# Kernel tuning notes

Measured on AMD Instinct MI355X. Metric: run time of the kernel, lower is better.

## Reference

```python
import jax, jax.numpy as jnp
import numpy as np

B, N, D, D_OUT = 8, 2048, 1024, 1024

def setup_inputs() -> dict:
    key = jax.random.key(0)
    k1, k2, k3, k4, k5 = jax.random.split(key, 5)
    x = jax.random.normal(k1, (B, N, D), dtype=jnp.float32)
    # nn.Linear params: weight [out, in], bias [out]
    W_attn = jax.random.normal(k2, (D, D), dtype=jnp.float32) / np.sqrt(D)
    b_attn = jax.random.normal(k3, (D,), dtype=jnp.float32) * 0.01
    W_out = jax.random.normal(k4, (D_OUT, D), dtype=jnp.float32) / np.sqrt(D)
    b_out = jax.random.normal(k5, (D_OUT,), dtype=jnp.float32) * 0.01
    return {"x": x, "W_attn": W_attn, "b_attn": b_attn, "W_out": W_out, "b_out": b_out}

def reference(x, W_attn, b_attn, W_out, b_out):
    # query = x; key = attention_linear(x); value = output_linear(x)
    key = jnp.einsum('bnd,kd->bnk', x, W_attn) + b_attn   # [B,N,D]
    value = jnp.einsum('bnd,od->bno', x, W_out) + b_out   # [B,N,D_OUT]
    scale = 1.0 / np.sqrt(x.shape[-1]).astype(np.float32)
    scores = jnp.einsum('bqd,bkd->bqk', x, key) * scale   # [B,N,N]
    attn = jax.nn.softmax(scores, axis=-1)
    return jnp.einsum('bqk,bko->bqo', attn, value)        # [B,N,D_OUT]
```

## Files before the change

### kernel.cpp

```cpp
#include <hip/hip_runtime.h>
#include <hip/hip_bf16.h>
#include <cstdio>

typedef __bf16 bf16_t;
typedef __bf16 bf16x8 __attribute__((ext_vector_type(8)));
typedef __bf16 bf16x4 __attribute__((ext_vector_type(4)));
typedef float  f32x16 __attribute__((ext_vector_type(16)));

#define TILE_E (256 * 64)

__global__ __launch_bounds__(256)
void cvt_all(const float* __restrict__ x,  bf16_t* __restrict__ xb,  int nX,
             const float* __restrict__ Wa, bf16_t* __restrict__ Wab,
             const float* __restrict__ Wo, bf16_t* __restrict__ Wob, int nW)
{
    const int nT = nX + 2 * nW;
    for (int i = (blockIdx.x * 256 + threadIdx.x) * 4; i < nT; i += gridDim.x * 256 * 4) {
        const float* src; bf16_t* dst; int off;
        if (i < nX)            { src = x;  dst = xb;  off = i; }
        else if (i < nX + nW)  { src = Wa; dst = Wab; off = i - nX; }
        else                   { src = Wo; dst = Wob; off = i - nX - nW; }
        const float4 v = *(const float4*)(src + off);
        bf16x4 o;
        o[0] = (bf16_t)v.x; o[1] = (bf16_t)v.y; o[2] = (bf16_t)v.z; o[3] = (bf16_t)v.w;
        *(bf16x4*)(dst + off) = o;
    }
}


template<int K>
__device__ __forceinline__ void stage_half(
    const bf16_t* __restrict__ src, bf16_t* lds_tile,
    int half, int kt, int w, int l)
{
    const int r0 = half * 128 + w * 8 + (l >> 3);
    const int c8 = ((l & 7) ^ (l >> 3)) * 8;
#pragma unroll
    for (int rr = 0; rr < 2; rr++) {
        __builtin_amdgcn_global_load_lds(
            (const __attribute__((address_space(1))) void*)
                (src + (size_t)(r0 + rr * 64) * K + (size_t)kt * 64 + c8),
            (__attribute__((address_space(3))) void*)
                (lds_tile + (half * 128 + rr * 64 + w * 8) * 64),
            16, 0, 0);
    }
}

#define RDF_A(f, ks) (*(const bf16x8*)&sAc[(aoff + (f) * 32 + l31) * 64 + ((((ks) * 2 + l5) ^ lo7) * 8)])
#define RDF_B(f, ks) (*(const bf16x8*)&sBc[(boff + (f) * 32 + l31) * 64 + ((((ks) * 2 + l5) ^ lo7) * 8)])

#define MFMA_QUAD(BV, MB, NB)                                              \
    _Pragma("unroll") for (int ks = 0; ks < 4; ks++)                       \
    _Pragma("unroll") for (int mi = 0; mi < 2; mi++)                       \
        acc[(MB) + mi][NB] = __builtin_amdgcn_mfma_f32_32x32x16_bf16(      \
            ar[mi][ks], BV[ks], acc[(MB) + mi][NB], 0, 0, 0);

#define LGKM0_FENCE                                        \
    asm volatile("s_waitcnt lgkmcnt(0)" ::: "memory");     \
    __builtin_amdgcn_sched_barrier(0);

template<int K>
__device__ __forceinline__ void gemm256_core(
    const bf16_t* __restrict__ Ab, const bf16_t* __restrict__ Bb,
    f32x16 (&acc)[4][2], int w, int l, int wm, int wn)
{
    __shared__ bf16_t sA[2 * TILE_E];
    __shared__ bf16_t sB[2 * TILE_E];
    constexpr int NKT = K / 64;

    const int l31 = l & 31, l5 = l >> 5, lo7 = l & 7;
    const int aoff = wm * 128, boff = wn * 64;

    stage_half<K>(Ab, sA, 0, 0, w, l);
    stage_half<K>(Bb, sB, 0, 0, w, l);
    stage_half<K>(Bb, sB, 1, 0, w, l);
    stage_half<K>(Ab, sA, 1, 0, w, l);
    stage_half<K>(Ab, sA + TILE_E, 0, 1, w, l);
    stage_half<K>(Bb, sB + TILE_E, 0, 1, w, l);
    stage_half<K>(Bb, sB + TILE_E, 1, 1, w, l);

    bf16x8 ar[2][4], bl[4], bh[4];

#pragma unroll 2
    for (int t = 0; t < NKT; ++t) {
        bf16_t* sAc = sA + (t & 1) * TILE_E;
        bf16_t* sBc = sB + (t & 1) * TILE_E;
        bf16_t* sAn = sA + ((t + 1) & 1) * TILE_E;

        if (t + 1 < NKT) { asm volatile("s_waitcnt vmcnt(6)" ::: "memory"); }
        else             { asm volatile("s_waitcnt vmcnt(0)" ::: "memory"); }
        __builtin_amdgcn_s_barrier();

#pragma unroll
        for (int mi = 0; mi < 2; mi++)
#pragma unroll
            for (int ks = 0; ks < 4; ks++) ar[mi][ks] = RDF_A(mi, ks);
#pragma unroll
        for (int ks = 0; ks < 4; ks++) bl[ks] = RDF_B(0, ks);
        if (t + 1 < NKT) stage_half<K>(Ab, sAn, 1, t + 1, w, l);
        __builtin_amdgcn_s_barrier();
        LGKM0_FENCE
        __builtin_amdgcn_s_setprio(1);
        MFMA_QUAD(bl, 0, 0)
        __builtin_amdgcn_s_setprio(0);
        __builtin_amdgcn_s_barrier();

#pragma unroll
        for (int ks = 0; ks < 4; ks++) bh[ks] = RDF_B(1, ks);
        __builtin_amdgcn_s_barrier();
        LGKM0_FENCE
        __builtin_amdgcn_s_setprio(1);
        MFMA_QUAD(bh, 0, 1)
        __builtin_amdgcn_s_setprio(0);
        __builtin_amdgcn_s_barrier();

#pragma unroll
        for (int mi = 0; mi < 2; mi++)
#pragma unroll
            for (int ks = 0; ks < 4; ks++) ar[mi][ks] = RDF_A(2 + mi, ks);
        if (t + 2 < NKT) stage_half<K>(Bb, sBc, 0, t + 2, w, l);
        __builtin_amdgcn_s_barrier();
        LGKM0_FENCE
        __builtin_amdgcn_s_setprio(1);
        MFMA_QUAD(bl, 2, 0)
        __builtin_amdgcn_s_setprio(0);
        __builtin_amdgcn_s_barrier();

        if (t + 2 < NKT) {
            stage_half<K>(Ab, sAc, 0, t + 2, w, l);
            stage_half<K>(Bb, sBc, 1, t + 2, w, l);
        }
        __builtin_amdgcn_s_barrier();
        __builtin_amdgcn_s_setprio(1);
        MFMA_QUAD(bh, 2, 1)
        __builtin_amdgcn_s_setprio(0);
        __builtin_amdgcn_s_barrier();
    }
}

#define ACC_INIT(acc)                                            \
    _Pragma("unroll") for (int i = 0; i < 4; i++)                \
    _Pragma("unroll") for (int j = 0; j < 2; j++)                \
    _Pragma("unroll") for (int e = 0; e < 16; e++) acc[i][j][e] = 0.f;

__global__ __launch_bounds__(512, 2)
void gemm_kv8(const bf16_t* __restrict__ xb,
              const bf16_t* __restrict__ Wa, const bf16_t* __restrict__ Wo,
              const float* __restrict__ ba, const float* __restrict__ bo,
              bf16_t* __restrict__ key, bf16_t* __restrict__ vT)
{
    constexpr int K = 1024, Nn = 2048, Dd = 1024;
    const int tid = threadIdx.x;
    const int w = tid >> 6, l = tid & 63;
    const int wm = w >> 2, wn = w & 3;

    const int bid = blockIdx.x;
    const int id  = (bid & 7) * 64 + (bid >> 3);
    const int b   = id >> 6;
    const int rest = id & 63;
    const int tm  = rest & 7;
    const int tn  = rest >> 3;
    const bool isK = tn < 4;

    const bf16_t* Ab = xb + (size_t)b * Nn * K + (size_t)tm * 256 * K;
    const bf16_t* Bb = isK ? (Wa + (size_t)tn * 256 * K)
                           : (Wo + (size_t)(tn - 4) * 256 * K);

    f32x16 acc[4][2];
    ACC_INIT(acc)
    gemm256_core<K>(Ab, Bb, acc, w, l, wm, wn);

    const int l31 = l & 31, l5 = l >> 5;
    if (isK) {
#pragma unroll
        for (int n = 0; n < 2; n++) {
            const int cg = (tn & 3) * 256 + wn * 64 + n * 32 + l31;
            const float bv = ba[cg];
#pragma unroll
            for (int m = 0; m < 4; m++)
#pragma unroll
                for (int rg = 0; rg < 4; rg++) {
                    const int rowg = tm * 256 + wm * 128 + m * 32 + rg * 8 + 4 * l5;
                    bf16_t* p = key + (size_t)b * Nn * Dd + (size_t)rowg * Dd + cg;
#pragma unroll
                    for (int j = 0; j < 4; j++)
                        p[(size_t)j * Dd] = (bf16_t)(acc[m][n][rg * 4 + j] + bv);
                }
        }
    } else {
#pragma unroll
        for (int n = 0; n < 2; n++) {
            const int cg = (tn & 3) * 256 + wn * 64 + n * 32 + l31;
            const float bv = bo[cg];
#pragma unroll
            for (int m = 0; m < 4; m++)
#pragma unroll
                for (int rg = 0; rg < 4; rg++) {
                    const int rowg = tm * 256 + wm * 128 + m * 32 + rg * 8 + 4 * l5;
                    bf16x4 pk;
#pragma unroll
                    for (int j = 0; j < 4; j++) pk[j] = (bf16_t)(acc[m][n][rg * 4 + j] + bv);
                    *(bf16x4*)(vT + (size_t)b * Dd * Nn + (size_t)cg * Nn + rowg) = pk;
                }
        }
    }
}

__global__ __launch_bounds__(512, 2)
void gemm_scores8(const bf16_t* __restrict__ xb, const bf16_t* __restrict__ key,
                  bf16_t* __restrict__ S)
{
    constexpr int K = 1024, Nn = 2048;
    const int tid = threadIdx.x;
    const int w = tid >> 6, l = tid & 63;
    const int wm = w >> 2, wn = w & 3;

    const int bid = blockIdx.x;
    const int id  = (bid & 7) * 64 + (bid >> 3);
    const int b   = id >> 6;
    const int rest = id & 63;
    const int tm  = rest & 7;
    const int tn  = rest >> 3;

    const bf16_t* Ab = xb  + (size_t)b * Nn * K + (size_t)tm * 256 * K;
    const bf16_t* Bb = key + (size_t)b * Nn * K + (size_t)tn * 256 * K;

    f32x16 acc[4][2];
    ACC_INIT(acc)
    gemm256_core<K>(Ab, Bb, acc, w, l, wm, wn);

    const int l31 = l & 31, l5 = l >> 5;
#pragma unroll
    for (int n = 0; n < 2; n++) {
        const int cg = tn * 256 + wn * 64 + n * 32 + l31;
#pragma unroll
        for (int m = 0; m < 4; m++)
#pragma unroll
            for (int rg = 0; rg < 4; rg++) {
                const int rowg = tm * 256 + wm * 128 + m * 32 + rg * 8 + 4 * l5;
                bf16_t* p = S + (size_t)b * Nn * Nn + (size_t)rowg * Nn + cg;
#pragma unroll
                for (int j = 0; j < 4; j++)
                    p[(size_t)j * Nn] = (bf16_t)(acc[m][n][rg * 4 + j] * 0.03125f);
            }
    }
}

__global__ __launch_bounds__(256)
void softmax_rows(bf16_t* __restrict__ S)
{
    __shared__ float red[8];
    const int t = threadIdx.x;
    const int w = t >> 6;
    const int lane = t & 63;
    bf16_t* p = S + (size_t)blockIdx.x * 2048;

    bf16x8 v = *(const bf16x8*)&p[t * 8];
    float x[8];
    float m = -1e30f;
#pragma unroll
    for (int i = 0; i < 8; i++) { x[i] = (float)v[i]; m = fmaxf(m, x[i]); }
#pragma unroll
    for (int off = 32; off >= 1; off >>= 1) m = fmaxf(m, __shfl_xor(m, off));
    if (lane == 0) red[w] = m;
    __syncthreads();
    m = fmaxf(fmaxf(red[0], red[1]), fmaxf(red[2], red[3]));

    float s = 0.f;
#pragma unroll
    for (int i = 0; i < 8; i++) { x[i] = __expf(x[i] - m); s += x[i]; }
#pragma unroll
    for (int off = 32; off >= 1; off >>= 1) s += __shfl_xor(s, off);
    if (lane == 0) red[4 + w] = s;
    __syncthreads();
    const float inv = 1.f / (red[4] + red[5] + red[6] + red[7]);

    bf16x8 o;
#pragma unroll
    for (int i = 0; i < 8; i++) o[i] = (bf16_t)(x[i] * inv);
    *(bf16x8*)&p[t * 8] = o;
}

__global__ __launch_bounds__(512, 2)
void gemm_out8(const bf16_t* __restrict__ P, const bf16_t* __restrict__ vT,
               float* __restrict__ out)
{
    constexpr int K = 2048, Nn = 2048, Dd = 1024;
    const int tid = threadIdx.x;
    const int w = tid >> 6, l = tid & 63;
    const int wm = w >> 2, wn = w & 3;

    const int bid = blockIdx.x;
    const int id  = (bid & 7) * 32 + (bid >> 3);
    const int b   = id >> 5;
    const int rest = id & 31;
    const int tm  = rest & 7;
    const int tn  = rest >> 3;

    const bf16_t* Ab = P  + (size_t)b * Nn * Nn + (size_t)tm * 256 * Nn;
    const bf16_t* Bb = vT + (size_t)b * Dd * Nn + (size_t)tn * 256 * Nn;

    f32x16 acc[4][2];
    ACC_INIT(acc)
    gemm256_core<K>(Ab, Bb, acc, w, l, wm, wn);

    const int l31 = l & 31, l5 = l >> 5;
#pragma unroll
    for (int n = 0; n < 2; n++) {
        const int cg = tn * 256 + wn * 64 + n * 32 + l31;
#pragma unroll
        for (int m = 0; m < 4; m++)
#pragma unroll
            for (int rg = 0; rg < 4; rg++) {
                const int rowg = tm * 256 + wm * 128 + m * 32 + rg * 8 + 4 * l5;
                float* p = out + (size_t)b * Nn * Dd + (size_t)rowg * Dd + cg;
#pragma unroll
                for (int j = 0; j < 4; j++)
                    p[(size_t)j * Dd] = acc[m][n][rg * 4 + j];
            }
    }
}

extern "C" void kernel_launch(void* const* d_in, const int* in_sizes, int n_in,
                              void* d_out, int out_size, void* d_ws, size_t ws_size,
                              hipStream_t stream)
{
    const int Bn = 8, Nn = 2048, Dd = 1024;

    const float* x  = (const float*)d_in[0];
    const float* Wa = (const float*)d_in[1];
    const float* ba = (const float*)d_in[2];
    const float* Wo = (const float*)d_in[3];
    const float* bo = (const float*)d_in[4];
    float* out = (float*)d_out;

    const size_t nX = (size_t)Bn * Nn * Dd;
    const size_t nW = (size_t)Dd * Dd;
    const size_t nS = (size_t)Bn * Nn * Nn;

    bf16_t* xb  = (bf16_t*)d_ws;
    bf16_t* Wab = xb + nX;
    bf16_t* Wob = Wab + nW;
    bf16_t* key = Wob + nW;
    bf16_t* vT  = key + nX;
    bf16_t* S   = vT + nX;
    const size_t needed = (nX * 3 + nW * 2 + nS) * sizeof(bf16_t);
    if (ws_size < needed)
        fprintf(stderr, "kernel_launch: ws too small: have %zu need %zu\n", ws_size, needed);

    cvt_all<<<dim3(18432), dim3(256), 0, stream>>>(x, xb, (int)nX, Wa, Wab, Wo, Wob, (int)nW);

    gemm_kv8<<<dim3(512), dim3(512), 0, stream>>>(xb, Wab, Wob, ba, bo, key, vT);

    gemm_scores8<<<dim3(512), dim3(512), 0, stream>>>(xb, key, S);

    softmax_rows<<<dim3(Bn * Nn), dim3(256), 0, stream>>>(S);

    gemm_out8<<<dim3(256), dim3(512), 0, stream>>>(S, vT, out);
}
```

Baseline: 377.3 us.

## Prefetch next LDS fragments during MFMA and change LDS swizzle pattern

Restructures the GEMM main loop so the next B-high and A-lower fragment reads from LDS are issued before the current MFMA block, using double register buffers (arA/arB) to overlap LDS reads with matrix math. The vmcnt wait and barrier move to the end of the iteration, and one barrier per phase is removed. It also changes the XOR swizzle of the staged tiles to include wave-dependent bits, to reduce LDS bank conflicts on reads. The cost is more vector registers and more delicate barrier and wait ordering, which could cause races or lower occupancy.

```diff
diff --git a/kernel.cpp b/kernel.cpp
--- a/kernel.cpp
+++ b/kernel.cpp
@@ -34,7 +34,7 @@
     int half, int kt, int w, int l)
 {
     const int r0 = half * 128 + w * 8 + (l >> 3);
-    const int c8 = ((l & 7) ^ (l >> 3)) * 8;
+    const int c8 = ((l & 7) ^ (l >> 3) ^ ((w & 3) << 1)) * 8;
 #pragma unroll
     for (int rr = 0; rr < 2; rr++) {
         __builtin_amdgcn_global_load_lds(
@@ -46,14 +46,14 @@
     }
 }
 
-#define RDF_A(f, ks) (*(const bf16x8*)&sAc[(aoff + (f) * 32 + l31) * 64 + ((((ks) * 2 + l5) ^ lo7) * 8)])
-#define RDF_B(f, ks) (*(const bf16x8*)&sBc[(boff + (f) * 32 + l31) * 64 + ((((ks) * 2 + l5) ^ lo7) * 8)])
-
-#define MFMA_QUAD(BV, MB, NB)                                              \
+#define RDF_A(f, ks) (*(const bf16x8*)&sAc[(aoff + (f) * 32 + l31) * 64 + ((((ks) * 2 + l5) ^ swz) * 8)])
+#define RDF_B(f, ks) (*(const bf16x8*)&sBc[(boff + (f) * 32 + l31) * 64 + ((((ks) * 2 + l5) ^ swz) * 8)])
+
+#define MFMA_Q(AR, BV, MB, NB)                                             \
     _Pragma("unroll") for (int ks = 0; ks < 4; ks++)                       \
     _Pragma("unroll") for (int mi = 0; mi < 2; mi++)                       \
         acc[(MB) + mi][NB] = __builtin_amdgcn_mfma_f32_32x32x16_bf16(      \
-            ar[mi][ks], BV[ks], acc[(MB) + mi][NB], 0, 0, 0);
+            AR[mi][ks], BV[ks], acc[(MB) + mi][NB], 0, 0, 0);
 
 #define LGKM0_FENCE                                        \
     asm volatile("s_waitcnt lgkmcnt(0)" ::: "memory");     \
@@ -68,7 +68,8 @@
     __shared__ bf16_t sB[2 * TILE_E];
     constexpr int NKT = K / 64;
 
-    const int l31 = l & 31, l5 = l >> 5, lo7 = l & 7;
+    const int l31 = l & 31, l5 = l >> 5;
+    const int swz = (l & 7) ^ ((l >> 2) & 6);
     const int aoff = wm * 128, boff = wn * 64;
 
     stage_half<K>(Ab, sA, 0, 0, w, l);
@@ -79,7 +80,10 @@
     stage_half<K>(Bb, sB + TILE_E, 0, 1, w, l);
     stage_half<K>(Bb, sB + TILE_E, 1, 1, w, l);
 
-    bf16x8 ar[2][4], bl[4], bh[4];
+    asm volatile("s_waitcnt vmcnt(6)" ::: "memory");
+    __builtin_amdgcn_s_barrier();
+
+    bf16x8 arA[2][4], arB[2][4], bl[4], bh[4];
 
 #pragma unroll 2
     for (int t = 0; t < NKT; ++t) {
@@ -87,42 +91,39 @@
         bf16_t* sBc = sB + (t & 1) * TILE_E;
         bf16_t* sAn = sA + ((t + 1) & 1) * TILE_E;
 
-        if (t + 1 < NKT) { asm volatile("s_waitcnt vmcnt(6)" ::: "memory"); }
-        else             { asm volatile("s_waitcnt vmcnt(0)" ::: "memory"); }
-        __builtin_amdgcn_s_barrier();
-
 #pragma unroll
         for (int mi = 0; mi < 2; mi++)
 #pragma unroll
-            for (int ks = 0; ks < 4; ks++) ar[mi][ks] = RDF_A(mi, ks);
+            for (int ks = 0; ks < 4; ks++) arA[mi][ks] = RDF_A(mi, ks);
 #pragma unroll
         for (int ks = 0; ks < 4; ks++) bl[ks] = RDF_B(0, ks);
         if (t + 1 < NKT) stage_half<K>(Ab, sAn, 1, t + 1, w, l);
         __builtin_amdgcn_s_barrier();
         LGKM0_FENCE
+#pragma unroll
+        for (int ks = 0; ks < 4; ks++) bh[ks] = RDF_B(1, ks);
+        __builtin_amdgcn_sched_barrier(0);
         __builtin_amdgcn_s_setprio(1);
-        MFMA_QUAD(bl, 0, 0)
+        MFMA_Q(arA, bl, 0, 0)
         __builtin_amdgcn_s_setprio(0);
         __builtin_amdgcn_s_barrier();
 
-#pragma unroll
-        for (int ks = 0; ks < 4; ks++) bh[ks] = RDF_B(1, ks);
+        LGKM0_FENCE
+#pragma unroll
+        for (int mi = 0; mi < 2; mi++)
+#pragma unroll
+            for (int ks = 0; ks < 4; ks++) arB[mi][ks] = RDF_A(2 + mi, ks);
+        __builtin_amdgcn_sched_barrier(0);
+        __builtin_amdgcn_s_setprio(1);
+        MFMA_Q(arA, bh, 0, 1)
+        __builtin_amdgcn_s_setprio(0);
+        __builtin_amdgcn_s_barrier();
+
+        if (t + 2 < NKT) stage_half<K>(Bb, sBc, 0, t + 2, w, l);
         __builtin_amdgcn_s_barrier();
         LGKM0_FENCE
         __builtin_amdgcn_s_setprio(1);
-        MFMA_QUAD(bh, 0, 1)
-        __builtin_amdgcn_s_setprio(0);
-        __builtin_amdgcn_s_barrier();
-
-#pragma unroll
-        for (int mi = 0; mi < 2; mi++)
-#pragma unroll
-            for (int ks = 0; ks < 4; ks++) ar[mi][ks] = RDF_A(2 + mi, ks);
-        if (t + 2 < NKT) stage_half<K>(Bb, sBc, 0, t + 2, w, l);
-        __builtin_amdgcn_s_barrier();
-        LGKM0_FENCE
-        __builtin_amdgcn_s_setprio(1);
-        MFMA_QUAD(bl, 2, 0)
+        MFMA_Q(arB, bl, 2, 0)
         __builtin_amdgcn_s_setprio(0);
         __builtin_amdgcn_s_barrier();
 
@@ -132,9 +133,15 @@
         }
         __builtin_amdgcn_s_barrier();
         __builtin_amdgcn_s_setprio(1);
-        MFMA_QUAD(bh, 2, 1)
+        MFMA_Q(arB, bh, 2, 1)
         __builtin_amdgcn_s_setprio(0);
-        __builtin_amdgcn_s_barrier();
+        if (t + 2 < NKT) {
+            asm volatile("s_waitcnt vmcnt(6)" ::: "memory");
+            __builtin_amdgcn_s_barrier();
+        } else if (t + 1 < NKT) {
+            asm volatile("s_waitcnt vmcnt(0)" ::: "memory");
+            __builtin_amdgcn_s_barrier();
+        }
     }
 }
 
```

Measured after the change: 400.6 us. +6.2%, slower.
